# Kernel tuning notes

Hardware: AMD Instinct MI355X
Metric: run time of the kernel (lower is better)

Reference implementation:

```python
import jax, jax.numpy as jnp
import numpy as np

NMS_THRE = 0.4
NEG = -1e30  # sentinel for sort key of suppressed boxes


def _iou_adjacency(boxes, nms_thre):
    # boxes: [N,4] in cxcywh -> xyxy, then dense IoU >= thre adjacency (no self loops)
    cx, cy, w, h = boxes[:, 0], boxes[:, 1], boxes[:, 2], boxes[:, 3]
    x1 = cx - w / 2
    y1 = cy - h / 2
    x2 = x1 + w
    y2 = y1 + h
    b = jnp.stack([x1, y1, x2, y2], axis=-1)  # [N,4]
    area = (x2 - x1) * (y2 - y1)
    lt = jnp.maximum(b[:, None, :2], b[None, :, :2])  # [N,N,2]
    rb = jnp.minimum(b[:, None, 2:], b[None, :, 2:])
    wh = jnp.clip(rb - lt, 0.0)
    inter = wh[..., 0] * wh[..., 1]
    iou = inter / (area[:, None] + area[None, :] - inter)
    n = boxes.shape[0]
    return (iou >= nms_thre) & (~jnp.eye(n, dtype=bool))


def _greedy_suppress(valid0, adj, scores):
    # Sequential greedy NMS over candidates in descending score order.
    # valid shrinks monotonically, and valid <= valid0 always, so clearing
    # neighbors via adj row exactly matches the torch loop (which only clears
    # neighbors that were initially valid -- already-false entries are no-ops).
    order = jnp.argsort(-scores)

    def body(k, valid):
        idx = order[k]
        return jnp.where(valid[idx], valid & (~adj[idx]), valid)

    return jax.lax.fori_loop(0, scores.shape[0], body, valid0)


def _per_class(pro_c, con_c, conf_c, adj):
    # scatter_max over adjacency: max of con over neighbors (0 if no neighbors,
    # matching torch_scatter's zero-init)
    adj_con = jnp.max(jnp.where(adj, con_c[None, :], 0.0), axis=1)
    valid0 = (pro_c >= conf_c) & (pro_c >= adj_con) & (pro_c >= con_c)
    return _greedy_suppress(valid0, adj, pro_c)


def _per_image(pro, con, boxes, scale, conf_thres):
    # pro/con: [N,C]; boxes: [N,4] cxcywh; scale: scalar; conf_thres: [C]
    adj = _iou_adjacency(boxes, NMS_THRE)
    survive = jax.vmap(_per_class, in_axes=(1, 1, 0, None))(pro, con, conf_thres, adj)  # [C,N]
    b = boxes * scale
    cx, cy, w, h = b[:, 0], b[:, 1], b[:, 2], b[:, 3]
    xyxy = jnp.stack([cx - 0.5 * w, cy - 0.5 * h, cx + 0.5 * w, cy + 0.5 * h], axis=-1)  # [N,4]
    scores = pro.T  # [C,N]
    C = scores.shape[0]
    bws = jnp.concatenate(
        [jnp.broadcast_to(xyxy[None], (C,) + xyxy.shape), scores[..., None]], axis=-1
    )  # [C,N,5]
    bws = bws * survive[..., None].astype(bws.dtype)  # zero out suppressed rows
    key = jnp.where(survive, scores, NEG)
    perm = jnp.argsort(-key, axis=1)  # per-class descending score order
    bws = jnp.take_along_axis(bws, perm[..., None], axis=1)
    mask = jnp.take_along_axis(survive, perm, axis=1)
    return bws, mask


def setup_inputs() -> dict:
    key = jax.random.key(0)
    k1, k2, k3, k4 = jax.random.split(key, 4)
    B, N, C = 4, 3600, 16
    return {
        "pro_max": jax.random.uniform(k1, (B, N, C), dtype=jnp.float32),
        "con_max": jax.random.uniform(k2, (B, N, C), dtype=jnp.float32),
        "pred_boxes": jax.random.uniform(k3, (B, N, 4), dtype=jnp.float32),
        "image_scales": jax.random.uniform(k4, (B,), dtype=jnp.float32),
        "conf_thres": jnp.zeros((C,), dtype=jnp.float32),
    }


def reference(pro_max, con_max, pred_boxes, image_scales, conf_thres):
    # Returns (boxes_with_scores [B,C,N,5] sorted per class by score desc,
    #          survive_mask [B,C,N] aligned with the sorted rows).
    return jax.vmap(_per_image, in_axes=(0, 0, 0, 0, None))(
        pro_max, con_max, pred_boxes, image_scales, conf_thres
    )
```

## Files before the change

### kernel.cpp

```cpp
#include <hip/hip_runtime.h>
#include <cstdint>

typedef unsigned long long u64;
typedef unsigned int u32;

#define B_ 4
#define N_ 3600
#define C_ 16
#define NW_ 57
#define NPAD_ 3648
#define RPW_ 4
#define RPB_ 16
#define TPI_ 1596
#define HW0_ 1856
#define HW1_ 1792
#define CH_ 64
#define NT_ 512
#define NWV_ 8
#define RPWG_ 8

__global__ __launch_bounds__(256, 4) void k_adj(const float* __restrict__ boxes,
                                                u64* __restrict__ adj) {
#pragma clang fp contract(off)
    __shared__ float4 sbox[HW0_];
    const int tid  = threadIdx.x;
    const int lane = tid & 63;
    const int wv   = tid >> 6;
    const int g    = blockIdx.x;
    const int b    = g / (N_ / RPB_);
    const int rg   = g % (N_ / RPB_);
    const int r0   = rg * RPB_ + wv * RPW_;
    const int w0   = rg >> 2;
    const size_t bN = (size_t)b * N_;

    float4 bi[RPW_];
    float  ai[RPW_];
#pragma unroll
    for (int r = 0; r < RPW_; ++r) {
        const float4 bx = reinterpret_cast<const float4*>(boxes)[bN + r0 + r];
        const float x1 = bx.x - bx.z * 0.5f;
        const float y1 = bx.y - bx.w * 0.5f;
        const float x2 = x1 + bx.z;
        const float y2 = y1 + bx.w;
        bi[r] = make_float4(x1, y1, x2, y2);
        ai[r] = (x2 - x1) * (y2 - y1);
    }
    const double MID = (double)0.4f - 0x1p-26;

    u64 row[RPW_];
#pragma unroll
    for (int r = 0; r < RPW_; ++r) row[r] = 0ull;

    int jbase = 0;
    for (int h = 0; h < 2; ++h) {
        const int cnt  = h ? HW1_ : HW0_;
        const int wlo  = jbase >> 6;
        const int wcnt = cnt >> 6;
        if (w0 < wlo + wcnt) {
            const int tw0 = max(w0 - wlo, 0);
            const int jj0 = tw0 << 6;
            __syncthreads();
            for (int jj = jj0 + tid; jj < cnt; jj += 256) {
                const int j = jbase + jj;
                float x1 = 0.f, y1 = 0.f, x2 = 0.f, y2 = 0.f;
                if (j < N_) {
                    const float4 bx = reinterpret_cast<const float4*>(boxes)[bN + j];
                    x1 = bx.x - bx.z * 0.5f;
                    y1 = bx.y - bx.w * 0.5f;
                    x2 = x1 + bx.z;
                    y2 = y1 + bx.w;
                }
                sbox[jj] = make_float4(x1, y1, x2, y2);
            }
            __syncthreads();

            for (int tw = tw0; tw < wcnt; ++tw) {
                const int tglob = wlo + tw;
                const float4 bj = sbox[tw * 64 + lane];
                const float ajr = (bj.z - bj.x) * (bj.w - bj.y);
#pragma unroll
                for (int r = 0; r < RPW_; ++r) {
                    const float ltx = fmaxf(bi[r].x, bj.x);
                    const float lty = fmaxf(bi[r].y, bj.y);
                    const float rbx = fminf(bi[r].z, bj.z);
                    const float rby = fminf(bi[r].w, bj.w);
                    const float whx = fmaxf(rbx - ltx, 0.0f);
                    const float why = fmaxf(rby - lty, 0.0f);
                    const float inter = whx * why;
                    const float denom = (ai[r] + ajr) - inter;
                    const int pred = ((double)inter > MID * (double)denom);
                    const u64 m = __ballot(pred);
                    if (lane == tglob) row[r] = m;
                }
            }
        }
        jbase += cnt;
    }

#pragma unroll
    for (int r = 0; r < RPW_; ++r)
        if (lane == w0) row[r] &= ~(1ull << ((r0 + r) & 63));

#pragma unroll
    for (int r = 0; r < RPW_; ++r)
        if (lane >= w0 && lane < NW_)
            adj[(bN + r0 + r) * (size_t)NW_ + lane] = row[r];
}

__global__ __launch_bounds__(256) void k_tr(u64* __restrict__ adj,
                                            u32* __restrict__ cnt) {
    if (blockIdx.x == 0) {
        for (int x = threadIdx.x; x < B_ * C_ * 16; x += 256) cnt[x] = 0;
    }
    const int lane = threadIdx.x & 63;
    const int wv   = threadIdx.x >> 6;
    const int p    = blockIdx.x * 4 + wv;
    const int b    = p / TPI_;
    const int p2   = p % TPI_;
    int wi = (int)((1.0f + sqrtf((float)(8 * p2 + 1))) * 0.5f);
    while (wi * (wi - 1) / 2 > p2) --wi;
    while ((wi + 1) * wi / 2 <= p2) ++wi;
    const int wj = p2 - wi * (wi - 1) / 2;
    const size_t bN = (size_t)b * N_;

    u64 x = adj[(bN + wj * 64 + lane) * (size_t)NW_ + wi];

    const u64 M[6] = {0x00000000FFFFFFFFull, 0x0000FFFF0000FFFFull,
                      0x00FF00FF00FF00FFull, 0x0F0F0F0F0F0F0F0Full,
                      0x3333333333333333ull, 0x5555555555555555ull};
#pragma unroll
    for (int si = 0; si < 6; ++si) {
        const int s = 32 >> si;
        const u64 m = M[si];
        const u64 t = __shfl_xor(x, s);
        x = ((lane & s) == 0) ? ((x & m) | ((t & m) << s))
                              : ((x & ~m) | ((t & ~m) >> s));
    }

    const int rowi = wi * 64 + lane;
    if (rowi < N_)
        adj[(bN + rowi) * (size_t)NW_ + wj] = x;
}

__global__ __launch_bounds__(256) void k_acon(const u64* __restrict__ adj,
                                              const float* __restrict__ con,
                                              const float* __restrict__ pro,
                                              const float* __restrict__ conf,
                                              u64* __restrict__ cand,
                                              u32* __restrict__ cnt) {
    const int tid  = threadIdx.x;
    const int lane = tid & 63;
    const int wv   = tid >> 6;
    const int g    = blockIdx.x;
    const int b    = g / (N_ / 4);
    const int i    = (g % (N_ / 4)) * 4 + wv;
    const size_t bN = (size_t)b * N_;

    u64 w = (lane < NW_) ? adj[(bN + i) * (size_t)NW_ + lane] : 0ull;

    float cm[C_];
#pragma unroll
    for (int k = 0; k < C_; ++k) cm[k] = 0.0f;

    while (w) {
        const int bit = __builtin_ctzll(w); w &= w - 1;
        const int j   = lane * 64 + bit;
        const float4* cp = reinterpret_cast<const float4*>(con + (bN + j) * C_);
        const float4 c0 = cp[0], c1 = cp[1], c2 = cp[2], c3 = cp[3];
        cm[0]  = fmaxf(cm[0],  c0.x); cm[1]  = fmaxf(cm[1],  c0.y);
        cm[2]  = fmaxf(cm[2],  c0.z); cm[3]  = fmaxf(cm[3],  c0.w);
        cm[4]  = fmaxf(cm[4],  c1.x); cm[5]  = fmaxf(cm[5],  c1.y);
        cm[6]  = fmaxf(cm[6],  c1.z); cm[7]  = fmaxf(cm[7],  c1.w);
        cm[8]  = fmaxf(cm[8],  c2.x); cm[9]  = fmaxf(cm[9],  c2.y);
        cm[10] = fmaxf(cm[10], c2.z); cm[11] = fmaxf(cm[11], c2.w);
        cm[12] = fmaxf(cm[12], c3.x); cm[13] = fmaxf(cm[13], c3.y);
        cm[14] = fmaxf(cm[14], c3.z); cm[15] = fmaxf(cm[15], c3.w);
    }

#pragma unroll
    for (int off = 1; off < 64; off <<= 1) {
#pragma unroll
        for (int k = 0; k < C_; ++k) cm[k] = fmaxf(cm[k], __shfl_xor(cm[k], off));
    }
    if (lane == 0) {
        const float4* cp = reinterpret_cast<const float4*>(con + (bN + i) * C_);
        const float4 c0 = cp[0], c1 = cp[1], c2 = cp[2], c3 = cp[3];
        const float4* pp = reinterpret_cast<const float4*>(pro + (bN + i) * C_);
        const float4 p0 = pp[0], p1 = pp[1], p2 = pp[2], p3 = pp[3];
        const float4* fp = reinterpret_cast<const float4*>(conf);
        const float4 f0 = fp[0], f1 = fp[1], f2 = fp[2], f3 = fp[3];
        const float th[C_] = {
            fmaxf(cm[0],  c0.x), fmaxf(cm[1],  c0.y),
            fmaxf(cm[2],  c0.z), fmaxf(cm[3],  c0.w),
            fmaxf(cm[4],  c1.x), fmaxf(cm[5],  c1.y),
            fmaxf(cm[6],  c1.z), fmaxf(cm[7],  c1.w),
            fmaxf(cm[8],  c2.x), fmaxf(cm[9],  c2.y),
            fmaxf(cm[10], c2.z), fmaxf(cm[11], c2.w),
            fmaxf(cm[12], c3.x), fmaxf(cm[13], c3.y),
            fmaxf(cm[14], c3.z), fmaxf(cm[15], c3.w)};
        const float pr[C_] = {p0.x, p0.y, p0.z, p0.w, p1.x, p1.y, p1.z, p1.w,
                              p2.x, p2.y, p2.z, p2.w, p3.x, p3.y, p3.z, p3.w};
        const float cf[C_] = {f0.x, f0.y, f0.z, f0.w, f1.x, f1.y, f1.z, f1.w,
                              f2.x, f2.y, f2.z, f2.w, f3.x, f3.y, f3.z, f3.w};
#pragma unroll
        for (int k = 0; k < C_; ++k) {
            if (pr[k] >= cf[k] && pr[k] >= th[k]) {
                const u32 pb = __float_as_uint(pr[k]);
                const u32 pk = pb ^ ((pb >> 31) ? 0xFFFFFFFFu : 0x80000000u);
                const u32 pos = atomicAdd(&cnt[(b * C_ + k) * 16], 1u);
                cand[(size_t)(b * C_ + k) * N_ + pos] =
                    (((u64)(~pk)) << 32) | (u32)i;
            }
        }
    }
}

union OvT {
    u64 keys[NPAD_];
    u64 srows[2][CH_][NW_];
};

__global__ __launch_bounds__(NT_) void k_nms(const u64* __restrict__ cand,
                                             const u32* __restrict__ cnt,
                                             const u64* __restrict__ adj,
                                             const float* __restrict__ boxes,
                                             const float* __restrict__ scales,
                                             float* __restrict__ out) {
#pragma clang fp contract(off)
    __shared__ OvT ov;
    __shared__ u32 sidx[NPAD_];
    __shared__ float sscore[NPAD_];
    __shared__ u64 sintra[CH_];
    __shared__ u64 vmask[NW_];
    __shared__ u64 s_accept;
    __shared__ u32 slist[NPAD_];
    __shared__ float slistf[NPAD_];
    __shared__ u32 s_S;
    const int tid  = threadIdx.x;
    const int lane = tid & 63;
    const int wv   = tid >> 6;
    const int bc   = blockIdx.x;
    const int b    = bc / C_;
    const size_t bN = (size_t)b * N_;

    const int T  = (int)cnt[bc * 16];
    const int TW = (T + 63) >> 6;
    for (int x = tid; x < TW * 64; x += NT_)
        ov.keys[x] = (x < T) ? cand[(size_t)bc * N_ + x] : ~0ull;
    if (tid < NW_) vmask[tid] = 0ull;
    __syncthreads();

    for (int xp = 0; xp * NT_ < T; ++xp) {
        const int x  = xp * NT_ + tid;
        const u64 kx = (x < T) ? ov.keys[x] : ~0ull;
        u32 rank = 0;
        for (int yb = 0; yb < TW; ++yb) {
            const u64 ky = ov.keys[yb * 64 + lane];
            const u32 kyl = (u32)ky, kyh = (u32)(ky >> 32);
#pragma unroll
            for (int l = 0; l < 64; ++l) {
                const u64 kb =
                    ((u64)(u32)__builtin_amdgcn_readlane((int)kyh, l) << 32)
                  |  (u64)(u32)__builtin_amdgcn_readlane((int)kyl, l);
                rank += (kb < kx) ? 1u : 0u;
            }
        }
        if (x < T) {
            const u32 i = (u32)(kx & 0xFFFFFFFFull);
            sidx[rank] = i;
            const u32 pk = ~((u32)(kx >> 32));
            const u32 pb = (pk & 0x80000000u) ? (pk ^ 0x80000000u) : ~pk;
            sscore[rank] = __uint_as_float(pb);
            atomicOr(&vmask[i >> 6], 1ull << (i & 63));
        }
    }
    __syncthreads();

#pragma unroll
    for (int rr = 0; rr < RPWG_; ++rr) {
        const int r = wv * RPWG_ + rr;
        const u32 idx = (r < T) ? sidx[r] : 0u;
        if (lane < NW_) ov.srows[0][r][lane] = adj[(bN + idx) * (size_t)NW_ + lane];
    }
    __syncthreads();

    u32 S = 0;
    const int NCH = (T + CH_ - 1) / CH_;
    for (int ch = 0; ch < NCH; ++ch) {
        const int cur = ch & 1, nxt = cur ^ 1;
        const int c0 = ch * CH_;
        const int cn = min(CH_, T - c0);
        const int havenext = (ch + 1 < NCH);

        u64 pre[RPWG_];
#pragma unroll
        for (int rr = 0; rr < RPWG_; ++rr) {
            const int r = wv * RPWG_ + rr;
            const int q = c0 + CH_ + r;
            const u32 idxn = (havenext && q < T) ? sidx[q] : 0u;
            pre[rr] = (havenext && lane < NW_)
                        ? adj[(bN + idxn) * (size_t)NW_ + lane] : 0ull;
        }
#pragma unroll
        for (int rr = 0; rr < RPWG_; ++rr) {
            const int r = wv * RPWG_ + rr;
            const u32 idxr = (c0 + r < T) ? sidx[c0 + r] : 0u;
            const u64 rj = ov.srows[cur][lane][idxr >> 6];
            const u64 ib = __ballot((lane < cn) && ((rj >> (idxr & 63)) & 1ull));
            if (lane == 0) sintra[r] = ib;
        }
        __syncthreads();

        if (wv == 0) {
            const u32 idxme = (c0 + lane < T) ? sidx[c0 + lane] : 0u;
            const u64 vm = vmask[idxme >> 6];
            u64 cv = __ballot((lane < cn) && ((vm >> (idxme & 63)) & 1ull));
            const u64 iv = sintra[lane];
            const u32 ivLo = (u32)iv, ivHi = (u32)(iv >> 32);
            u64 accept = 0ull;
            while (cv) {
                const int r = __builtin_ctzll(cv);
                accept |= 1ull << r;
                const u64 ir =
                    ((u64)(u32)__builtin_amdgcn_readlane((int)ivHi, r) << 32)
                  |  (u64)(u32)__builtin_amdgcn_readlane((int)ivLo, r);
                cv &= ~(ir | (1ull << r));
            }
            if (lane == 0) s_accept = accept;
            const u32 bitl = (u32)((accept >> lane) & 1ull);
            if (bitl) {
                const u32 pos = S + (u32)__popcll(accept & ((1ull << lane) - 1ull));
                slist[pos]  = idxme;
                slistf[pos] = sscore[c0 + lane];
            }
            S += (u32)__popcll(accept);
        }
        __syncthreads();

        const u64 ac = s_accept;
        u64 acc = 0ull;
#pragma unroll
        for (int rr = 0; rr < RPWG_; ++rr) {
            const int r = wv * RPWG_ + rr;
            if ((ac >> r) & 1ull)
                acc |= ov.srows[cur][r][min(lane, NW_ - 1)];
        }
        if (lane < NW_ && acc)
            atomicAnd(&vmask[lane], ~acc);
        if (havenext) {
#pragma unroll
            for (int rr = 0; rr < RPWG_; ++rr) {
                const int r = wv * RPWG_ + rr;
                if (lane < NW_) ov.srows[nxt][r][lane] = pre[rr];
            }
        }
        __syncthreads();
    }
    if (wv == 0 && lane == 0) s_S = S;
    __syncthreads();

    const int Sf = (int)s_S;
    const float s = scales[b];
    for (int r = tid; r < N_; r += NT_) {
        float o0 = 0.f, o1 = 0.f, o2 = 0.f, o3 = 0.f, o4 = 0.f, mk = 0.f;
        if (r < Sf) {
            const int idx = (int)slist[r];
            const float4 bx = reinterpret_cast<const float4*>(boxes)[bN + idx];
            const float scx = bx.x * s, scy = bx.y * s;
            const float sw  = bx.z * s, sh  = bx.w * s;
            o0 = scx - 0.5f * sw;
            o1 = scy - 0.5f * sh;
            o2 = scx + 0.5f * sw;
            o3 = scy + 0.5f * sh;
            o4 = slistf[r];
            mk = 1.0f;
        }
        float* o = out + ((size_t)bc * N_ + r) * 5;
        o[0] = o0; o[1] = o1; o[2] = o2; o[3] = o3; o[4] = o4;
        out[(size_t)B_ * C_ * N_ * 5 + (size_t)bc * N_ + r] = mk;
    }
}

extern "C" void kernel_launch(void* const* d_in, const int* in_sizes, int n_in,
                              void* d_out, int out_size, void* d_ws, size_t ws_size,
                              hipStream_t stream) {
    const float* pro    = (const float*)d_in[0];
    const float* con    = (const float*)d_in[1];
    const float* boxes  = (const float*)d_in[2];
    const float* scales = (const float*)d_in[3];
    const float* conf   = (const float*)d_in[4];

    char* ws = (char*)d_ws;
    u64* adj = (u64*)ws;
    size_t off = (size_t)B_ * N_ * NW_ * sizeof(u64);
    u64* cand = (u64*)(ws + off);
    off += (size_t)B_ * C_ * N_ * sizeof(u64);
    u32* cnt = (u32*)(ws + off);

    k_adj <<<B_ * N_ / RPB_, 256, 0, stream>>>(boxes, adj);
    k_tr  <<<B_ * TPI_ / 4,  256, 0, stream>>>(adj, cnt);
    k_acon<<<B_ * N_ / 4,    256, 0, stream>>>(adj, con, pro, conf, cand, cnt);
    k_nms <<<B_ * C_,        NT_, 0, stream>>>(cand, cnt, adj, boxes,
                                               scales, (float*)d_out);
}
```

Measured before the change: 170.7 us.

## Split NMS output writing into separate wide kernel and parallelize intra-chunk greedy

The sequential per-chunk greedy loop, which accepted one candidate per iteration via readlane, now accepts in each round every candidate with no surviving higher-ranked conflict, OR-reducing their suppression masks with shuffles. The final output formatting, which ran inside only 64 blocks, moves to a new kernel over all B*C*N rows. The NMS kernel stores its survivor lists and counts to workspace instead. This adds a kernel launch plus a workspace round trip, and each round of the new loop costs a 6-step shuffle reduction.

```diff
diff --git a/kernel.cpp b/kernel.cpp
--- a/kernel.cpp
+++ b/kernel.cpp
@@ -100,7 +100,6 @@
 #pragma unroll
     for (int r = 0; r < RPW_; ++r)
         if (lane == w0) row[r] &= ~(1ull << ((r0 + r) & 63));
-
 #pragma unroll
     for (int r = 0; r < RPW_; ++r)
         if (lane >= w0 && lane < NW_)
@@ -136,7 +135,6 @@
         x = ((lane & s) == 0) ? ((x & m) | ((t & m) << s))
                               : ((x & ~m) | ((t & ~m) >> s));
     }
-
     const int rowi = wi * 64 + lane;
     if (rowi < N_)
         adj[(bN + rowi) * (size_t)NW_ + wj] = x;
@@ -220,12 +218,12 @@
     u64 srows[2][CH_][NW_];
 };
 
-__global__ __launch_bounds__(NT_) void k_nms(const u64* __restrict__ cand,
-                                             const u32* __restrict__ cnt,
-                                             const u64* __restrict__ adj,
-                                             const float* __restrict__ boxes,
-                                             const float* __restrict__ scales,
-                                             float* __restrict__ out) {
+__global__ __launch_bounds__(NT_) void k_nms_core(const u64* __restrict__ cand,
+                                                  const u32* __restrict__ cnt,
+                                                  const u64* __restrict__ adj,
+                                                  u32* __restrict__ scnt,
+                                                  u32* __restrict__ sl,
+                                                  float* __restrict__ sf) {
 #pragma clang fp contract(off)
     __shared__ OvT ov;
     __shared__ u32 sidx[NPAD_];
@@ -280,7 +278,8 @@
     for (int rr = 0; rr < RPWG_; ++rr) {
         const int r = wv * RPWG_ + rr;
         const u32 idx = (r < T) ? sidx[r] : 0u;
-        if (lane < NW_) ov.srows[0][r][lane] = adj[(bN + idx) * (size_t)NW_ + lane];
+        if (lane < NW_)
+            ov.srows[0][r][lane] = adj[(bN + idx) * (size_t)NW_ + lane];
     }
     __syncthreads();
 
@@ -316,20 +315,22 @@
             const u64 vm = vmask[idxme >> 6];
             u64 cv = __ballot((lane < cn) && ((vm >> (idxme & 63)) & 1ull));
             const u64 iv = sintra[lane];
-            const u32 ivLo = (u32)iv, ivHi = (u32)(iv >> 32);
+            const u64 below = (1ull << lane) - 1ull;
             u64 accept = 0ull;
             while (cv) {
-                const int r = __builtin_ctzll(cv);
-                accept |= 1ull << r;
-                const u64 ir =
-                    ((u64)(u32)__builtin_amdgcn_readlane((int)ivHi, r) << 32)
-                  |  (u64)(u32)__builtin_amdgcn_readlane((int)ivLo, r);
-                cv &= ~(ir | (1ull << r));
+                const int ok = ((cv >> lane) & 1ull) &&
+                               ((iv & below & cv) == 0ull);
+                const u64 ar = __ballot(ok);
+                u64 sup = ok ? iv : 0ull;
+#pragma unroll
+                for (int off = 1; off < 64; off <<= 1)
+                    sup |= __shfl_xor(sup, off);
+                accept |= ar;
+                cv &= ~(ar | sup);
             }
             if (lane == 0) s_accept = accept;
-            const u32 bitl = (u32)((accept >> lane) & 1ull);
-            if (bitl) {
-                const u32 pos = S + (u32)__popcll(accept & ((1ull << lane) - 1ull));
+            if ((accept >> lane) & 1ull) {
+                const u32 pos = S + (u32)__popcll(accept & below);
                 slist[pos]  = idxme;
                 slistf[pos] = sscore[c0 + lane];
             }
@@ -356,29 +357,48 @@
         }
         __syncthreads();
     }
-    if (wv == 0 && lane == 0) s_S = S;
+    if (wv == 0 && lane == 0) { s_S = S; scnt[bc] = S; }
     __syncthreads();
 
     const int Sf = (int)s_S;
-    const float s = scales[b];
-    for (int r = tid; r < N_; r += NT_) {
-        float o0 = 0.f, o1 = 0.f, o2 = 0.f, o3 = 0.f, o4 = 0.f, mk = 0.f;
-        if (r < Sf) {
-            const int idx = (int)slist[r];
-            const float4 bx = reinterpret_cast<const float4*>(boxes)[bN + idx];
-            const float scx = bx.x * s, scy = bx.y * s;
-            const float sw  = bx.z * s, sh  = bx.w * s;
-            o0 = scx - 0.5f * sw;
-            o1 = scy - 0.5f * sh;
-            o2 = scx + 0.5f * sw;
-            o3 = scy + 0.5f * sh;
-            o4 = slistf[r];
-            mk = 1.0f;
-        }
-        float* o = out + ((size_t)bc * N_ + r) * 5;
-        o[0] = o0; o[1] = o1; o[2] = o2; o[3] = o3; o[4] = o4;
-        out[(size_t)B_ * C_ * N_ * 5 + (size_t)bc * N_ + r] = mk;
-    }
+    for (int r = tid; r < Sf; r += NT_) {
+        sl[(size_t)bc * N_ + r] = slist[r];
+        sf[(size_t)bc * N_ + r] = slistf[r];
+    }
+}
+
+__global__ __launch_bounds__(512) void k_out(const u32* __restrict__ scnt,
+                                             const u32* __restrict__ sl,
+                                             const float* __restrict__ sf,
+                                             const float* __restrict__ boxes,
+                                             const float* __restrict__ scales,
+                                             float* __restrict__ out) {
+#pragma clang fp contract(off)
+    const int x = blockIdx.x * 512 + threadIdx.x;
+    if (x >= B_ * C_ * N_) return;
+    const int bc = x / N_;
+    const int r  = x - bc * N_;
+    const int b  = bc / C_;
+    const int S  = (int)scnt[bc];
+
+    float o0 = 0.f, o1 = 0.f, o2 = 0.f, o3 = 0.f, o4 = 0.f, mk = 0.f;
+    if (r < S) {
+        const int idx = (int)sl[(size_t)bc * N_ + r];
+        const float4 bx =
+            reinterpret_cast<const float4*>(boxes)[(size_t)b * N_ + idx];
+        const float s = scales[b];
+        const float scx = bx.x * s, scy = bx.y * s;
+        const float sw  = bx.z * s, sh  = bx.w * s;
+        o0 = scx - 0.5f * sw;
+        o1 = scy - 0.5f * sh;
+        o2 = scx + 0.5f * sw;
+        o3 = scy + 0.5f * sh;
+        o4 = sf[(size_t)bc * N_ + r];
+        mk = 1.0f;
+    }
+    float* o = out + (size_t)x * 5;
+    o[0] = o0; o[1] = o1; o[2] = o2; o[3] = o3; o[4] = o4;
+    out[(size_t)B_ * C_ * N_ * 5 + x] = mk;
 }
 
 extern "C" void kernel_launch(void* const* d_in, const int* in_sizes, int n_in,
@@ -396,10 +416,17 @@
     u64* cand = (u64*)(ws + off);
     off += (size_t)B_ * C_ * N_ * sizeof(u64);
     u32* cnt = (u32*)(ws + off);
-
-    k_adj <<<B_ * N_ / RPB_, 256, 0, stream>>>(boxes, adj);
-    k_tr  <<<B_ * TPI_ / 4,  256, 0, stream>>>(adj, cnt);
-    k_acon<<<B_ * N_ / 4,    256, 0, stream>>>(adj, con, pro, conf, cand, cnt);
-    k_nms <<<B_ * C_,        NT_, 0, stream>>>(cand, cnt, adj, boxes,
-                                               scales, (float*)d_out);
-}
+    off += (size_t)B_ * C_ * 16 * sizeof(u32);
+    u32* scnt = (u32*)(ws + off);
+    off += (size_t)B_ * C_ * sizeof(u32);
+    u32* sl = (u32*)(ws + off);
+    off += (size_t)B_ * C_ * N_ * sizeof(u32);
+    float* sf = (float*)(ws + off);
+
+    k_adj     <<<B_ * N_ / RPB_, 256, 0, stream>>>(boxes, adj);
+    k_tr      <<<B_ * TPI_ / 4,  256, 0, stream>>>(adj, cnt);
+    k_acon    <<<B_ * N_ / 4,    256, 0, stream>>>(adj, con, pro, conf, cand, cnt);
+    k_nms_core<<<B_ * C_,        NT_, 0, stream>>>(cand, cnt, adj, scnt, sl, sf);
+    k_out     <<<450,            512, 0, stream>>>(scnt, sl, sf, boxes, scales,
+                                                   (float*)d_out);
+}
```

Measured after the change: 161.4 us. -5.4%, faster.
